# Kernel optimization log

Measured on AMD Instinct MI355X. Metric: run time of the kernel, lower is better.

## Reference

```python
import jax, jax.numpy as jnp
import numpy as np

N_SIGMA = 1
NUM_CLASS = 1
N_INST = 16          # max instance id (ids 1..16); instances==0 is background
W_INST, W_VAR, W_SEED = 1.0, 10.0, 1.0
H, W, B = 512, 512, 8
GRID = 1024          # buffer is linspace over 1024 then cropped to H,W


def make_xym(h, w, dtype=jnp.float32):
    full = jnp.linspace(0.0, 1.0, GRID, dtype=dtype)
    xm = jnp.broadcast_to(full[:w][None, :], (h, w))   # x varies along width
    ym = jnp.broadcast_to(full[:h][:, None], (h, w))   # y varies along height
    return jnp.stack([xm, ym], axis=0)                 # [2, H, W]


def lovasz_hinge_flat(logits, labels):
    # logits: [N] float, labels: [N] float in {0,1}
    signs = 2.0 * labels - 1.0
    errors = 1.0 - logits * signs
    order = jnp.argsort(-errors)
    errors_sorted = errors[order]
    gt_sorted = labels[order]
    gts = jnp.sum(gt_sorted)
    intersection = gts - jnp.cumsum(gt_sorted)
    union = gts + jnp.cumsum(1.0 - gt_sorted)
    jaccard = 1.0 - intersection / union
    grad = jnp.concatenate([jaccard[:1], jaccard[1:] - jaccard[:-1]])
    return jnp.sum(jax.nn.relu(errors_sorted) * grad)


def _per_image(pred, instance, label, xym):
    h, w = pred.shape[1], pred.shape[2]
    spatial_emb = jnp.tanh(pred[0:2]) + xym              # [2,H,W]
    sigma = pred[2:2 + N_SIGMA]                          # [n_sigma,H,W]
    seed = jax.nn.sigmoid(pred[2 + N_SIGMA])             # [H,W] (num_class==1)

    label_mask = (label == 1)
    bg_mask = (label == 0)
    seed_loss = jnp.sum(jnp.where(bg_mask, seed ** 2, 0.0))

    ids = jnp.arange(1, N_INST + 1)
    masks = (instance[None] == ids[:, None, None]) & label_mask[None]  # [K,H,W] bool
    maskf = masks.astype(pred.dtype)
    counts = jnp.sum(maskf, axis=(1, 2))                 # [K]
    present = counts > 0
    safe = jnp.maximum(counts, 1.0)

    # to_center=True: center = mean of xym coords over each instance mask
    center = jnp.einsum('khw,chw->kc', maskf, xym) / safe[:, None]        # [K,2]
    s_mean = jnp.einsum('khw,shw->ks', maskf, sigma) / safe[:, None]      # [K,n_sigma]

    # var loss: mean over in-mask pixels of (sigma - detached mean)^2
    dev2 = (sigma[None] - jax.lax.stop_gradient(s_mean)[:, :, None, None]) ** 2  # [K,ns,H,W]
    var_terms = jnp.einsum('khw,kshw->k', maskf, dev2) / (safe * N_SIGMA)

    # dist = exp(-s * sum_c (emb_c - center_c)^2), s = exp(10 * mean sigma)
    s_exp = jnp.exp(10.0 * s_mean)[:, 0]                 # [K] (n_sigma==1 broadcasts)
    diff2 = jnp.sum((spatial_emb[None] - center[:, :, None, None]) ** 2, axis=1)  # [K,H,W]
    dist = jnp.exp(-s_exp[:, None, None] * diff2)        # [K,H,W]

    inst_losses = jax.vmap(
        lambda d, m: lovasz_hinge_flat(2.0 * d.ravel() - 1.0, m.ravel())
    )(dist, maskf)
    instance_loss = jnp.sum(jnp.where(present, inst_losses, 0.0))
    var_loss = jnp.sum(jnp.where(present, var_terms, 0.0))

    seed_loss = seed_loss + jnp.sum(
        maskf * (seed[None] - jax.lax.stop_gradient(dist)) ** 2)

    obj = jnp.maximum(jnp.sum(present.astype(pred.dtype)), 1.0)
    return (W_INST * instance_loss / obj
            + W_VAR * var_loss / obj
            + W_SEED * seed_loss / (h * w))


def setup_inputs() -> dict:
    key = jax.random.key(0)
    k1, k2, k3 = jax.random.split(key, 3)
    prediction = jax.random.normal(k1, (B, 2 + N_SIGMA + NUM_CLASS, H, W), dtype=jnp.float32)
    instances = jax.random.randint(k2, (B, H, W), 0, N_INST + 1).astype(jnp.int64)
    labels = jax.random.randint(k3, (B, H, W), 0, NUM_CLASS + 1).astype(jnp.int64)
    return {"prediction": prediction, "instances": instances, "labels": labels}


def reference(prediction, instances, labels):
    xym = make_xym(prediction.shape[2], prediction.shape[3], prediction.dtype)
    per_img = jax.vmap(_per_image, in_axes=(0, 0, 0, None))(
        prediction, instances, labels, xym)
    return jnp.mean(per_img)
```

## Files before the change

### kernel.cpp

```cpp
#include <hip/hip_runtime.h>
#include <hip/hip_fp16.h>
#include <math.h>

#define HWPX 262144
#define NIMG 8
#define ACC_STRIDE 96
#define NB 1024
#define ZMAX 8.0f
#define NSPLIT 16
#define NGRP 2
#define PREP_BLOCKS 256

typedef unsigned long long u64;

__device__ __forceinline__ float tanh_fast(float x) {
  float t = __expf(2.0f * x);
  return 1.0f - __fdividef(2.0f, t + 1.0f);
}
__device__ __forceinline__ float sigmoid_fast(float x) {
  return __fdividef(1.0f, 1.0f + __expf(-x));
}

template<bool PACK>
__global__ __launch_bounds__(1024) void k_prep(const float* __restrict__ pred,
    const int* __restrict__ inst, const int* __restrict__ lab,
    u64* __restrict__ rec, float* __restrict__ part)
{
  __shared__ float s[8][83];
  int t = threadIdx.x;
  for (int i = t; i < 8*83; i += 1024) (&s[0][0])[i] = 0.0f;
  __syncthreads();
  int bid = blockIdx.x;
  int b = bid >> 5;
  int chunk = bid & 31;
  const float* pb = pred + (size_t)b*4*HWPX;
  size_t ib = (size_t)b*HWPX;
  int r = t & 7;
  float bg = 0.0f;
  #pragma unroll
  for (int j = 0; j < 8; ++j) {
    int px = (chunk << 13) + (j << 10) + t;
    float X = pb[px];
    float Y = pb[HWPX + px];
    float Gv = pb[2*HWPX + px];
    float Q = pb[3*HWPX + px];
    int L = lab[ib + px];
    int I = inst[ib + px];
    int w = px & 511, h = px >> 9;
    float xm = (float)w * (1.0f/1023.0f), ym = (float)h * (1.0f/1023.0f);
    float sd = sigmoid_fast(Q);
    int mid = (L == 1 && (unsigned)(I-1) < 16u) ? I : 0;
    if (PACK) {
      float ex = tanh_fast(X) + xm;
      float ey = tanh_fast(Y) + ym;
      rec[ib + px] = (u64)__half_as_ushort(__float2half(ex))
                   | ((u64)__half_as_ushort(__float2half(ey)) << 16)
                   | ((u64)__half_as_ushort(__float2half(sd)) << 32)
                   | ((u64)mid << 48);
    }
    if (L == 0) {
      bg += sd*sd;
    } else if (mid) {
      int k = mid - 1;
      atomicAdd(&s[r][k], 1.0f);
      atomicAdd(&s[r][16+k], xm);
      atomicAdd(&s[r][32+k], ym);
      atomicAdd(&s[r][48+k], Gv);
      atomicAdd(&s[r][64+k], Gv*Gv);
    }
  }
  #pragma unroll
  for (int o = 32; o > 0; o >>= 1) bg += __shfl_down(bg, o);
  if ((t & 63) == 0) atomicAdd(&s[0][80], bg);
  __syncthreads();
  if (t < 96) {
    float v = 0.0f;
    if (t < 81) {
      #pragma unroll
      for (int rr = 0; rr < 8; ++rr) v += s[rr][t];
    }
    part[(size_t)bid*96 + t] = v;
  }
}

__global__ __launch_bounds__(128) void k_fin(const float* __restrict__ part,
    double* __restrict__ accd, float* __restrict__ pairinfo)
{
  __shared__ float red[96];
  int t = threadIdx.x, b = blockIdx.x;
  if (t < 96) {
    float v = 0.0f;
    const float* pp = part + (size_t)b*32*96 + t;
    #pragma unroll 8
    for (int blk = 0; blk < 32; ++blk) v += pp[(size_t)blk*96];
    red[t] = v;
  }
  __syncthreads();
  if (t < 16) {
    float cnt = red[t];
    float safe = cnt > 0.0f ? cnt : 1.0f;
    float sm = red[48+t] / safe;
    float4 pi = make_float4(red[16+t]/safe, red[32+t]/safe, __expf(10.0f*sm), cnt);
    ((float4*)pairinfo)[b*16 + t] = pi;
  }
  if (t == 0) {
    double vs = 0.0; float np = 0.0f;
    for (int k2 = 0; k2 < 16; ++k2) {
      float cnt = red[k2];
      if (cnt > 0.0f) {
        np += 1.0f;
        float ssg = red[48+k2];
        float var = (red[64+k2] - ssg*ssg/cnt) / cnt;
        if (var < 0.0f) var = 0.0f;
        vs += (double)var;
      }
    }
    double* ab = accd + (size_t)b*ACC_STRIDE;
    ab[80] = (double)red[80];
    ab[81] = 0.0;
    ab[82] = 0.0;
    ab[83] = vs;
    ab[84] = np > 1.0f ? (double)np : 1.0;
  }
}

__global__ __launch_bounds__(1024) void k_hist(const u64* __restrict__ rec,
    const float* __restrict__ pairinfo,
    unsigned* __restrict__ partial, double* __restrict__ accd)
{
  __shared__ unsigned hist[8*NB];
  __shared__ float redf[16];
  int t = threadIdx.x, bid = blockIdx.x;
  int b = bid & 7;
  int rr = bid >> 3;
  int g = rr & 1;
  int s = rr >> 1;
  for (int i = t; i < 8*NB; i += 1024) hist[i] = 0u;
  float cx[8], cy[8], se[8], s128[8];
  #pragma unroll
  for (int j = 0; j < 8; ++j) {
    float4 pi = ((const float4*)pairinfo)[b*16 + g*8 + j];
    cx[j] = pi.x; cy[j] = pi.y; se[j] = pi.z; s128[j] = pi.z * ((float)NB/ZMAX);
  }
  __syncthreads();
  size_t base = (size_t)b*HWPX + (size_t)s*(HWPX/NSPLIT);
  float fit = 0.0f;
  #pragma unroll 2
  for (int it = 0; it < HWPX/NSPLIT/1024; ++it) {
    size_t px = base + it*1024 + t;
    u64 v = rec[px];
    float ex = __half2float(__ushort_as_half((unsigned short)(v & 0xffffu)));
    float ey = __half2float(__ushort_as_half((unsigned short)((v >> 16) & 0xffffu)));
    float sd = __half2float(__ushort_as_half((unsigned short)((v >> 32) & 0xffffu)));
    int rel = (int)(v >> 48) - 1 - g*8;
    #pragma unroll
    for (int j = 0; j < 8; ++j) {
      float dx = ex - cx[j], dy = ey - cy[j];
      float d2 = fmaf(dx, dx, dy*dy);
      int key; unsigned add;
      if (rel == j) {
        float d = __expf(-d2 * se[j]);
        float e = fmaf(-2.0f, d, 2.0f);
        int kk = (int)(e * (float)(NB/2));
        key = kk > NB-1 ? NB-1 : kk;
        add = 0x10000u;
        float df = sd - d; fit += df*df;
      } else {
        key = (int)fminf(d2 * s128[j], (float)(NB-1));
        add = 1u;
      }
      atomicAdd(&hist[j*NB + key], add);
    }
  }
  #pragma unroll
  for (int o = 32; o > 0; o >>= 1) fit += __shfl_down(fit, o);
  if ((t & 63) == 0) redf[t >> 6] = fit;
  __syncthreads();
  if (t == 0) {
    float ft = 0.0f;
    for (int i = 0; i < 16; ++i) ft += redf[i];
    atomicAdd(&accd[(size_t)b*ACC_STRIDE + 81], (double)ft);
  }
  unsigned* pp = partial + (size_t)((b*NGRP + g)*NSPLIT + s)*(8*NB);
  for (int i = t; i < 8*NB; i += 1024) pp[i] = hist[i];
}

__global__ __launch_bounds__(1024) void k_scan(const unsigned* __restrict__ partial,
    const float* __restrict__ pairinfo, double* __restrict__ accd)
{
  __shared__ unsigned sp[NB], sq[NB];
  __shared__ float red[16];
  int t = threadIdx.x, bid = blockIdx.x;
  int b = bid >> 4, k = bid & 15;
  int g = k >> 3, j8 = k & 7;
  float G = pairinfo[(b*16 + k)*4 + 3];
  if (G <= 0.0f) return;
  sq[t] = 0u;
  __syncthreads();
  unsigned p = 0, q = 0;
  const unsigned* basep = partial + (size_t)((b*NGRP + g)*NSPLIT)*(8*NB) + j8*NB + t;
  #pragma unroll 4
  for (int s2 = 0; s2 < NSPLIT; ++s2) {
    unsigned h = basep[(size_t)s2*(8*NB)];
    p += h >> 16; q += h & 0xffffu;
  }
  float zmid = (t + 0.5f) * (ZMAX/NB);
  float ev = 2.0f * __expf(-zmid);
  int eb = (int)(ev * (float)(NB/2));
  if (eb > NB-1) eb = NB-1;
  if (q) atomicAdd(&sq[eb], q);
  __syncthreads();
  unsigned qe = sq[t];
  __syncthreads();
  int j = (NB-1) - t;
  sp[j] = p; sq[j] = qe;
  __syncthreads();
  for (int off = 1; off < NB; off <<= 1) {
    unsigned vp = 0, vq = 0;
    if (j >= off) { vp = sp[j-off]; vq = sq[j-off]; }
    __syncthreads();
    sp[j] += vp; sq[j] += vq;
    __syncthreads();
  }
  float A  = (float)(sp[j] - p);
  float Bn = (float)(sq[j] - qe);
  float val = (t + 0.5f) * (2.0f/NB);
  float pf = (float)p, qf = (float)qe;
  float Jb = (A + Bn) / (G + Bn);
  float Ja = (A + Bn + pf + qf) / (G + Bn + qf);
  float contrib = val * (Ja - Jb);
  #pragma unroll
  for (int o = 32; o > 0; o >>= 1) contrib += __shfl_down(contrib, o);
  if ((t & 63) == 0) red[t >> 6] = contrib;
  __syncthreads();
  if (t == 0) {
    float tot = 0.0f;
    for (int i = 0; i < 16; ++i) tot += red[i];
    atomicAdd(&accd[(size_t)b*ACC_STRIDE + 82], (double)tot);
  }
}

__global__ __launch_bounds__(1024) void k_lov_old(const float* __restrict__ pred,
    const int* __restrict__ inst, const int* __restrict__ lab,
    const float* __restrict__ pairinfo, double* __restrict__ accd)
{
  constexpr int SHIFT = 18;
  constexpr int NBB = (0x40000000 >> SHIFT) + 1;
  extern __shared__ unsigned char smem[];
  unsigned* histP = reinterpret_cast<unsigned*>(smem);
  unsigned* histQ = histP + NBB;
  unsigned* scanP = histQ + NBB;
  unsigned* scanQ = scanP + 1024;
  float* red  = reinterpret_cast<float*>(scanQ + 1024);
  float* redf = red + 16;
  int t = threadIdx.x, bid = blockIdx.x;
  int b = bid >> 4, k = bid & 15;
  float4 pi = reinterpret_cast<const float4*>(pairinfo)[bid];
  float cx = pi.x, cy = pi.y, sexp = pi.z, G = pi.w;
  if (G <= 0.0f) return;
  for (int i = t; i < 2*NBB; i += 1024) histP[i] = 0u;
  __syncthreads();
  size_t ib = (size_t)b * HWPX;
  const float* pb = pred + (size_t)b * 4 * HWPX;
  const int target = k + 1;
  float fit = 0.0f;
  for (int j = 0; j < HWPX/1024; ++j) {
    int px = (j << 10) + t;
    int h = px >> 9, w = px & 511;
    float ex = tanhf(pb[px]) + w*(1.0f/1023.0f);
    float ey = tanhf(pb[HWPX+px]) + h*(1.0f/1023.0f);
    float sd = 1.0f/(1.0f + __expf(-pb[3*HWPX+px]));
    int lv = lab[ib+px], iv = inst[ib+px];
    float dx = ex - cx, dy = ey - cy;
    float d = __expf(-sexp * (dx*dx + dy*dy));
    bool m = (lv == 1) && (iv == target);
    float e = m ? fmaf(-2.0f, d, 2.0f) : 2.0f * d;
    unsigned key = __float_as_uint(e) >> SHIFT;
    atomicAdd(m ? &histP[key] : &histQ[key], 1u);
    if (m) { float df = sd - d; fit += df*df; }
  }
  #pragma unroll
  for (int o = 32; o > 0; o >>= 1) fit += __shfl_down(fit, o);
  if ((t & 63) == 0) redf[t >> 6] = fit;
  __syncthreads();
  constexpr int CB = NBB / 1024;
  int start = (NBB - 1) - t * CB;
  int nk = (t == 1023) ? (CB + 1) : CB;
  unsigned lp = 0, lq = 0;
  for (int i = 0; i < nk; ++i) { lp += histP[start-i]; lq += histQ[start-i]; }
  scanP[t] = lp; scanQ[t] = lq;
  __syncthreads();
  for (int off = 1; off < 1024; off <<= 1) {
    unsigned vp = 0, vq = 0;
    if (t >= off) { vp = scanP[t-off]; vq = scanQ[t-off]; }
    __syncthreads();
    scanP[t] += vp; scanQ[t] += vq;
    __syncthreads();
  }
  float A  = (float)(scanP[t] - lp);
  float Bn = (float)(scanQ[t] - lq);
  float contrib = 0.0f;
  for (int i = 0; i < nk; ++i) {
    int kk = start - i;
    unsigned p = histP[kk], q = histQ[kk];
    if (p | q) {
      float lo = __uint_as_float((unsigned)kk << SHIFT);
      float hi = __uint_as_float((unsigned)(kk+1) << SHIFT);
      float valv = 0.5f*(lo+hi);
      if (valv > 2.0f) valv = 2.0f;
      float pq = (float)(p + q), qf = (float)q;
      float Jb = (A + Bn) / (G + Bn);
      float Ja = (A + Bn + pq) / (G + Bn + qf);
      contrib += valv * (Ja - Jb);
      A += (float)p; Bn += qf;
    }
  }
  #pragma unroll
  for (int o = 32; o > 0; o >>= 1) contrib += __shfl_down(contrib, o);
  if ((t & 63) == 0) red[t >> 6] = contrib;
  __syncthreads();
  if (t == 0) {
    float tot = 0.0f, ft = 0.0f;
    for (int i = 0; i < 16; ++i) { tot += red[i]; ft += redf[i]; }
    atomicAdd(&accd[(size_t)b*ACC_STRIDE + 82], (double)tot);
    atomicAdd(&accd[(size_t)b*ACC_STRIDE + 81], (double)ft);
  }
}

__global__ void k_final(const double* __restrict__ accd, float* __restrict__ out)
{
  int t = threadIdx.x;
  double lb = 0.0;
  if (t < NIMG) {
    const double* ab = accd + (size_t)t*ACC_STRIDE;
    lb = (ab[82] + 10.0*ab[83]) / ab[84] + (ab[80] + ab[81]) * (1.0/(double)HWPX);
  }
  #pragma unroll
  for (int o = 4; o > 0; o >>= 1) lb += __shfl_down(lb, o);
  if (t == 0) out[0] = (float)(lb * 0.125);
}

extern "C" void kernel_launch(void* const* d_in, const int* in_sizes, int n_in,
                              void* d_out, int out_size, void* d_ws, size_t ws_size,
                              hipStream_t stream)
{
  const float* pred = (const float*)d_in[0];
  const int*   inst = (const int*)d_in[1];
  const int*   lab  = (const int*)d_in[2];
  float* out = (float*)d_out;

  size_t recB   = (size_t)NIMG * HWPX * sizeof(u64);
  size_t partB  = (size_t)NIMG * NGRP * NSPLIT * 8 * NB * 4;
  size_t pstatB = (size_t)PREP_BLOCKS * 96 * sizeof(float);
  size_t accB   = (size_t)NIMG * ACC_STRIDE * sizeof(double);
  size_t pairB  = 128 * 4 * sizeof(float);
  bool full = ws_size >= recB + partB + pstatB + accB + pairB;

  char* ws = (char*)d_ws;
  if (full) {
    u64*      rec   = (u64*)ws;
    unsigned* part  = (unsigned*)(ws + recB);
    float*    pstat = (float*)(ws + recB + partB);
    double*   accd  = (double*)(ws + recB + partB + pstatB);
    float*    pairinfo = (float*)(ws + recB + partB + pstatB + accB);
    k_prep<true><<<PREP_BLOCKS,1024,0,stream>>>(pred, inst, lab, rec, pstat);
    k_fin<<<NIMG,128,0,stream>>>(pstat, accd, pairinfo);
    k_hist<<<NIMG*NGRP*NSPLIT,1024,0,stream>>>(rec, pairinfo, part, accd);
    k_scan<<<128,1024,0,stream>>>(part, pairinfo, accd);
    k_final<<<1,64,0,stream>>>(accd, out);
  } else {
    float*    pstat = (float*)ws;
    double*   accd  = (double*)(ws + pstatB);
    float*    pairinfo = (float*)(ws + pstatB + accB);
    k_prep<false><<<PREP_BLOCKS,1024,0,stream>>>(pred, inst, lab, nullptr, pstat);
    k_fin<<<NIMG,128,0,stream>>>(pstat, accd, pairinfo);
    size_t lds18 = ((size_t)2*4097 + 2048)*4 + 128;
    k_lov_old<<<128,1024,lds18,stream>>>(pred, inst, lab, pairinfo, accd);
    k_final<<<1,64,0,stream>>>(accd, out);
  }
}
```

Before: 65.70 us.

## Drop packed intermediate buffer; recompute embeddings in histogram kernel with 16 instances

The prep kernel no longer writes a packed half-precision per-pixel record. The stats kernel now reads only sigma, labels and instances. The histogram kernel reads the raw prediction and label inputs directly, recomputes tanh and sigmoid, and also accumulates the background seed loss. It handles all 16 instances per block with a 512-bin histogram and a 32-way pixel split, instead of two groups of 8 with 1024 bins. This removes a 16 MB write and read of intermediates, at the cost of re-reading the fp32/int inputs, doing more transcendental work per pixel, and coarser histogram quantization in the Lovasz approximation.

```diff
diff --git a/kernel.cpp b/kernel.cpp
--- a/kernel.cpp
+++ b/kernel.cpp
@@ -1,15 +1,13 @@
 #include <hip/hip_runtime.h>
-#include <hip/hip_fp16.h>
 #include <math.h>
 
 #define HWPX 262144
 #define NIMG 8
 #define ACC_STRIDE 96
-#define NB 1024
+#define NB 512
 #define ZMAX 8.0f
-#define NSPLIT 16
-#define NGRP 2
-#define PREP_BLOCKS 256
+#define NSPLIT 32
+#define STAT_BLOCKS 256
 
 typedef unsigned long long u64;
 
@@ -21,10 +19,9 @@
   return __fdividef(1.0f, 1.0f + __expf(-x));
 }
 
-template<bool PACK>
-__global__ __launch_bounds__(1024) void k_prep(const float* __restrict__ pred,
+__global__ __launch_bounds__(1024) void k_stats(const float* __restrict__ pred,
     const int* __restrict__ inst, const int* __restrict__ lab,
-    u64* __restrict__ rec, float* __restrict__ part)
+    float* __restrict__ part)
 {
   __shared__ float s[8][83];
   int t = threadIdx.x;
@@ -36,31 +33,16 @@
   const float* pb = pred + (size_t)b*4*HWPX;
   size_t ib = (size_t)b*HWPX;
   int r = t & 7;
-  float bg = 0.0f;
   #pragma unroll
   for (int j = 0; j < 8; ++j) {
     int px = (chunk << 13) + (j << 10) + t;
-    float X = pb[px];
-    float Y = pb[HWPX + px];
     float Gv = pb[2*HWPX + px];
-    float Q = pb[3*HWPX + px];
     int L = lab[ib + px];
     int I = inst[ib + px];
-    int w = px & 511, h = px >> 9;
-    float xm = (float)w * (1.0f/1023.0f), ym = (float)h * (1.0f/1023.0f);
-    float sd = sigmoid_fast(Q);
     int mid = (L == 1 && (unsigned)(I-1) < 16u) ? I : 0;
-    if (PACK) {
-      float ex = tanh_fast(X) + xm;
-      float ey = tanh_fast(Y) + ym;
-      rec[ib + px] = (u64)__half_as_ushort(__float2half(ex))
-                   | ((u64)__half_as_ushort(__float2half(ey)) << 16)
-                   | ((u64)__half_as_ushort(__float2half(sd)) << 32)
-                   | ((u64)mid << 48);
-    }
-    if (L == 0) {
-      bg += sd*sd;
-    } else if (mid) {
+    if (mid) {
+      int w = px & 511, h = px >> 9;
+      float xm = (float)w * (1.0f/1023.0f), ym = (float)h * (1.0f/1023.0f);
       int k = mid - 1;
       atomicAdd(&s[r][k], 1.0f);
       atomicAdd(&s[r][16+k], xm);
@@ -69,13 +51,10 @@
       atomicAdd(&s[r][64+k], Gv*Gv);
     }
   }
-  #pragma unroll
-  for (int o = 32; o > 0; o >>= 1) bg += __shfl_down(bg, o);
-  if ((t & 63) == 0) atomicAdd(&s[0][80], bg);
   __syncthreads();
   if (t < 96) {
     float v = 0.0f;
-    if (t < 81) {
+    if (t < 80) {
       #pragma unroll
       for (int rr = 0; rr < 8; ++rr) v += s[rr][t];
     }
@@ -116,7 +95,7 @@
       }
     }
     double* ab = accd + (size_t)b*ACC_STRIDE;
-    ab[80] = (double)red[80];
+    ab[80] = 0.0;
     ab[81] = 0.0;
     ab[82] = 0.0;
     ab[83] = vs;
@@ -124,84 +103,91 @@
   }
 }
 
-__global__ __launch_bounds__(1024) void k_hist(const u64* __restrict__ rec,
+__global__ __launch_bounds__(1024) void k_hist(const float* __restrict__ pred,
+    const int* __restrict__ inst, const int* __restrict__ lab,
     const float* __restrict__ pairinfo,
     unsigned* __restrict__ partial, double* __restrict__ accd)
 {
-  __shared__ unsigned hist[8*NB];
-  __shared__ float redf[16];
+  __shared__ unsigned hist[16*NB];
+  __shared__ float redf[16], redb[16];
   int t = threadIdx.x, bid = blockIdx.x;
   int b = bid & 7;
-  int rr = bid >> 3;
-  int g = rr & 1;
-  int s = rr >> 1;
-  for (int i = t; i < 8*NB; i += 1024) hist[i] = 0u;
-  float cx[8], cy[8], se[8], s128[8];
-  #pragma unroll
-  for (int j = 0; j < 8; ++j) {
-    float4 pi = ((const float4*)pairinfo)[b*16 + g*8 + j];
-    cx[j] = pi.x; cy[j] = pi.y; se[j] = pi.z; s128[j] = pi.z * ((float)NB/ZMAX);
-  }
-  __syncthreads();
-  size_t base = (size_t)b*HWPX + (size_t)s*(HWPX/NSPLIT);
-  float fit = 0.0f;
+  int s = bid >> 3;
+  for (int i = t; i < 16*NB; i += 1024) hist[i] = 0u;
+  float cx[16], cy[16], s128[16];
+  #pragma unroll
+  for (int j = 0; j < 16; ++j) {
+    float4 pi = ((const float4*)pairinfo)[b*16 + j];
+    cx[j] = pi.x; cy[j] = pi.y; s128[j] = pi.z * ((float)NB/ZMAX);
+  }
+  __syncthreads();
+  const float* pb = pred + (size_t)b*4*HWPX;
+  size_t ib = (size_t)b*HWPX;
+  float fit = 0.0f, bg = 0.0f;
   #pragma unroll 2
   for (int it = 0; it < HWPX/NSPLIT/1024; ++it) {
-    size_t px = base + it*1024 + t;
-    u64 v = rec[px];
-    float ex = __half2float(__ushort_as_half((unsigned short)(v & 0xffffu)));
-    float ey = __half2float(__ushort_as_half((unsigned short)((v >> 16) & 0xffffu)));
-    float sd = __half2float(__ushort_as_half((unsigned short)((v >> 32) & 0xffffu)));
-    int rel = (int)(v >> 48) - 1 - g*8;
+    int lpx = s*(HWPX/NSPLIT) + it*1024 + t;
+    float X = pb[lpx];
+    float Y = pb[HWPX + lpx];
+    float Q = pb[3*HWPX + lpx];
+    int L = lab[ib + lpx];
+    int I = inst[ib + lpx];
+    int w = lpx & 511, h = lpx >> 9;
+    float xm = (float)w * (1.0f/1023.0f), ym = (float)h * (1.0f/1023.0f);
+    float exf = tanh_fast(X) + xm;
+    float eyf = tanh_fast(Y) + ym;
+    float sd = sigmoid_fast(Q);
+    int rel = (L == 1 && (unsigned)(I-1) < 16u) ? (I-1) : -1;
+    bg += (L == 0) ? sd*sd : 0.0f;
     #pragma unroll
-    for (int j = 0; j < 8; ++j) {
-      float dx = ex - cx[j], dy = ey - cy[j];
-      float d2 = fmaf(dx, dx, dy*dy);
+    for (int j = 0; j < 16; ++j) {
+      float dx = exf - cx[j], dy = eyf - cy[j];
+      float z = fmaf(dx, dx, dy*dy) * s128[j];
       int key; unsigned add;
-      if (rel == j) {
-        float d = __expf(-d2 * se[j]);
+      if (j == rel) {
+        float d = __expf(-z * (ZMAX/(float)NB));
         float e = fmaf(-2.0f, d, 2.0f);
-        int kk = (int)(e * (float)(NB/2));
-        key = kk > NB-1 ? NB-1 : kk;
+        int kp = (int)(e * (float)(NB/2));
+        key = kp > NB-1 ? NB-1 : kp;
         add = 0x10000u;
         float df = sd - d; fit += df*df;
       } else {
-        key = (int)fminf(d2 * s128[j], (float)(NB-1));
+        key = (int)fminf(z, (float)(NB-1));
         add = 1u;
       }
       atomicAdd(&hist[j*NB + key], add);
     }
   }
   #pragma unroll
-  for (int o = 32; o > 0; o >>= 1) fit += __shfl_down(fit, o);
-  if ((t & 63) == 0) redf[t >> 6] = fit;
-  __syncthreads();
-  if (t == 0) {
-    float ft = 0.0f;
-    for (int i = 0; i < 16; ++i) ft += redf[i];
+  for (int o = 32; o > 0; o >>= 1) { fit += __shfl_down(fit, o); bg += __shfl_down(bg, o); }
+  if ((t & 63) == 0) { redf[t >> 6] = fit; redb[t >> 6] = bg; }
+  __syncthreads();
+  if (t == 0) {
+    float ft = 0.0f, bt = 0.0f;
+    for (int i = 0; i < 16; ++i) { ft += redf[i]; bt += redb[i]; }
     atomicAdd(&accd[(size_t)b*ACC_STRIDE + 81], (double)ft);
-  }
-  unsigned* pp = partial + (size_t)((b*NGRP + g)*NSPLIT + s)*(8*NB);
-  for (int i = t; i < 8*NB; i += 1024) pp[i] = hist[i];
-}
-
-__global__ __launch_bounds__(1024) void k_scan(const unsigned* __restrict__ partial,
+    atomicAdd(&accd[(size_t)b*ACC_STRIDE + 80], (double)bt);
+  }
+  unsigned* pp = partial + (size_t)(b*NSPLIT + s)*(16*NB);
+  for (int i = t; i < 16*NB; i += 1024) pp[i] = hist[i];
+}
+
+__global__ __launch_bounds__(NB) void k_scan(const unsigned* __restrict__ partial,
     const float* __restrict__ pairinfo, double* __restrict__ accd)
 {
   __shared__ unsigned sp[NB], sq[NB];
-  __shared__ float red[16];
+  __shared__ float red[8];
   int t = threadIdx.x, bid = blockIdx.x;
   int b = bid >> 4, k = bid & 15;
-  int g = k >> 3, j8 = k & 7;
   float G = pairinfo[(b*16 + k)*4 + 3];
   if (G <= 0.0f) return;
   sq[t] = 0u;
   __syncthreads();
   unsigned p = 0, q = 0;
-  const unsigned* basep = partial + (size_t)((b*NGRP + g)*NSPLIT)*(8*NB) + j8*NB + t;
+  const unsigned* basep = partial + (size_t)(b*NSPLIT)*(16*NB) + k*NB + t;
   #pragma unroll 4
   for (int s2 = 0; s2 < NSPLIT; ++s2) {
-    unsigned h = basep[(size_t)s2*(8*NB)];
+    unsigned h = basep[(size_t)s2*(16*NB)];
     p += h >> 16; q += h & 0xffffu;
   }
   float zmid = (t + 0.5f) * (ZMAX/NB);
@@ -235,8 +221,47 @@
   __syncthreads();
   if (t == 0) {
     float tot = 0.0f;
-    for (int i = 0; i < 16; ++i) tot += red[i];
+    for (int i = 0; i < NB/64; ++i) tot += red[i];
     atomicAdd(&accd[(size_t)b*ACC_STRIDE + 82], (double)tot);
+  }
+}
+
+__global__ void k_final(const double* __restrict__ accd, float* __restrict__ out)
+{
+  int t = threadIdx.x;
+  double lb = 0.0;
+  if (t < NIMG) {
+    const double* ab = accd + (size_t)t*ACC_STRIDE;
+    lb = (ab[82] + 10.0*ab[83]) / ab[84] + (ab[80] + ab[81]) * (1.0/(double)HWPX);
+  }
+  #pragma unroll
+  for (int o = 4; o > 0; o >>= 1) lb += __shfl_down(lb, o);
+  if (t == 0) out[0] = (float)(lb * 0.125);
+}
+
+__global__ __launch_bounds__(1024) void k_bg(const float* __restrict__ pred,
+    const int* __restrict__ lab, double* __restrict__ accd)
+{
+  __shared__ float redb[16];
+  int t = threadIdx.x, bid = blockIdx.x;
+  int b = bid >> 5, chunk = bid & 31;
+  const float* pb = pred + (size_t)b*4*HWPX;
+  size_t ib = (size_t)b*HWPX;
+  float bg = 0.0f;
+  #pragma unroll
+  for (int j = 0; j < 8; ++j) {
+    int px = (chunk << 13) + (j << 10) + t;
+    float sd = sigmoid_fast(pb[3*HWPX + px]);
+    bg += (lab[ib + px] == 0) ? sd*sd : 0.0f;
+  }
+  #pragma unroll
+  for (int o = 32; o > 0; o >>= 1) bg += __shfl_down(bg, o);
+  if ((t & 63) == 0) redb[t >> 6] = bg;
+  __syncthreads();
+  if (t == 0) {
+    float bt = 0.0f;
+    for (int i = 0; i < 16; ++i) bt += redb[i];
+    atomicAdd(&accd[(size_t)b*ACC_STRIDE + 80], (double)bt);
   }
 }
 
@@ -327,19 +352,6 @@
   }
 }
 
-__global__ void k_final(const double* __restrict__ accd, float* __restrict__ out)
-{
-  int t = threadIdx.x;
-  double lb = 0.0;
-  if (t < NIMG) {
-    const double* ab = accd + (size_t)t*ACC_STRIDE;
-    lb = (ab[82] + 10.0*ab[83]) / ab[84] + (ab[80] + ab[81]) * (1.0/(double)HWPX);
-  }
-  #pragma unroll
-  for (int o = 4; o > 0; o >>= 1) lb += __shfl_down(lb, o);
-  if (t == 0) out[0] = (float)(lb * 0.125);
-}
-
 extern "C" void kernel_launch(void* const* d_in, const int* in_sizes, int n_in,
                               void* d_out, int out_size, void* d_ws, size_t ws_size,
                               hipStream_t stream)
@@ -349,31 +361,30 @@
   const int*   lab  = (const int*)d_in[2];
   float* out = (float*)d_out;
 
-  size_t recB   = (size_t)NIMG * HWPX * sizeof(u64);
-  size_t partB  = (size_t)NIMG * NGRP * NSPLIT * 8 * NB * 4;
-  size_t pstatB = (size_t)PREP_BLOCKS * 96 * sizeof(float);
+  size_t partB  = (size_t)NIMG * NSPLIT * 16 * NB * 4;
+  size_t pstatB = (size_t)STAT_BLOCKS * 96 * sizeof(float);
   size_t accB   = (size_t)NIMG * ACC_STRIDE * sizeof(double);
   size_t pairB  = 128 * 4 * sizeof(float);
-  bool full = ws_size >= recB + partB + pstatB + accB + pairB;
+  bool full = ws_size >= partB + pstatB + accB + pairB;
 
   char* ws = (char*)d_ws;
   if (full) {
-    u64*      rec   = (u64*)ws;
-    unsigned* part  = (unsigned*)(ws + recB);
-    float*    pstat = (float*)(ws + recB + partB);
-    double*   accd  = (double*)(ws + recB + partB + pstatB);
-    float*    pairinfo = (float*)(ws + recB + partB + pstatB + accB);
-    k_prep<true><<<PREP_BLOCKS,1024,0,stream>>>(pred, inst, lab, rec, pstat);
+    unsigned* part  = (unsigned*)ws;
+    float*    pstat = (float*)(ws + partB);
+    double*   accd  = (double*)(ws + partB + pstatB);
+    float*    pairinfo = (float*)(ws + partB + pstatB + accB);
+    k_stats<<<STAT_BLOCKS,1024,0,stream>>>(pred, inst, lab, pstat);
     k_fin<<<NIMG,128,0,stream>>>(pstat, accd, pairinfo);
-    k_hist<<<NIMG*NGRP*NSPLIT,1024,0,stream>>>(rec, pairinfo, part, accd);
-    k_scan<<<128,1024,0,stream>>>(part, pairinfo, accd);
+    k_hist<<<NIMG*NSPLIT,1024,0,stream>>>(pred, inst, lab, pairinfo, part, accd);
+    k_scan<<<128,NB,0,stream>>>(part, pairinfo, accd);
     k_final<<<1,64,0,stream>>>(accd, out);
   } else {
     float*    pstat = (float*)ws;
     double*   accd  = (double*)(ws + pstatB);
     float*    pairinfo = (float*)(ws + pstatB + accB);
-    k_prep<false><<<PREP_BLOCKS,1024,0,stream>>>(pred, inst, lab, nullptr, pstat);
+    k_stats<<<STAT_BLOCKS,1024,0,stream>>>(pred, inst, lab, pstat);
     k_fin<<<NIMG,128,0,stream>>>(pstat, accd, pairinfo);
+    k_bg<<<STAT_BLOCKS,1024,0,stream>>>(pred, lab, accd);
     size_t lds18 = ((size_t)2*4097 + 2048)*4 + 128;
     k_lov_old<<<128,1024,lds18,stream>>>(pred, inst, lab, pairinfo, accd);
     k_final<<<1,64,0,stream>>>(accd, out);
```

New measurement: 67.33 us. 2.5% more time.
